# Kernel tuning notes

Hardware: AMD Instinct MI355X
Metric: run time of the kernel (lower is better)

The kernel has to match this reference:

```python
import jax, jax.numpy as jnp
import numpy as np
from functools import partial

NUM_HEADS = 12
NUM_CLUSTERS = 98
LN_EPS = 1e-5
INF = 1e10


def _ln(x, g, b):
    m = x.mean(-1, keepdims=True)
    v = ((x - m) ** 2).mean(-1, keepdims=True)
    return (x - m) / jnp.sqrt(v + LN_EPS) * g + b


def _agglom(dist, num_clusters):
    # dist: [T,T] precomputed distances; average-linkage agglomerative clustering.
    T = dist.shape[0]
    D = dist.at[jnp.arange(T), jnp.arange(T)].set(INF)
    sizes = jnp.ones((T,), dist.dtype)
    labels = jnp.arange(T)
    active = jnp.ones((T,), bool)

    def step(_, state):
        D, sizes, labels, active = state
        Dm = jnp.where(active[:, None] & active[None, :], D, INF)
        idx = jnp.argmin(Dm)
        i0, j0 = idx // T, idx % T
        i = jnp.minimum(i0, j0)
        j = jnp.maximum(i0, j0)
        ni, nj = sizes[i], sizes[j]
        # Lance-Williams update for average linkage
        newd = (ni * D[i] + nj * D[j]) / (ni + nj)
        D = D.at[i, :].set(newd).at[:, i].set(newd)
        D = D.at[i, i].set(INF)
        D = D.at[j, :].set(INF).at[:, j].set(INF)
        sizes = sizes.at[i].set(ni + nj)
        labels = jnp.where(labels == j, i, labels)
        active = active.at[j].set(False)
        return (D, sizes, labels, active)

    D, sizes, labels, active = jax.lax.fori_loop(0, T - num_clusters, step, (D, sizes, labels, active))
    rank = jnp.cumsum(active.astype(jnp.int32)) - 1  # compact active cluster ids to 0..K-1
    return rank[labels]


def reference(x, attn_size, n1_g, n1_b, w_qkv, w_proj, b_proj, n2_g, n2_b, w_fc1, b_fc1, w_fc2, b_fc2):
    B, N, C = x.shape
    H = NUM_HEADS
    hd = C // H
    # --- Attention_ToMe ---
    h = _ln(x, n1_g, n1_b)
    qkv = (h @ w_qkv).reshape(B, N, 3, H, hd).transpose(2, 0, 3, 1, 4)
    q, k, v = qkv[0], qkv[1], qkv[2]
    metric = k.mean(axis=1)  # [B,N,hd]
    attn = jnp.einsum('bhqd,bhkd->bhqk', q, k) * (hd ** -0.5)
    attn = attn + jnp.log(attn_size)[:, None, None, :, 0]  # size bias (log 1 = 0 first block)
    attn = jax.nn.softmax(attn, axis=-1)
    xa = jnp.einsum('bhqk,bhkd->bqhd', attn, v).reshape(B, N, C)
    x = x + xa @ w_proj + b_proj
    # --- agglomerative clustering (no_grad in original) ---
    m = jax.lax.stop_gradient(metric)
    m = m / jnp.linalg.norm(m, axis=-1, keepdims=True)
    dist = 1.0 - jnp.einsum('bnd,bmd->bnm', m, m)[:, 1:, 1:]  # drop cls token
    labels = jax.vmap(partial(_agglom, num_clusters=NUM_CLUSTERS))(dist)  # [B,N-1]
    labels = jnp.concatenate([jnp.zeros((B, 1), labels.dtype), labels + 1], axis=1)  # cls -> cluster 0
    # --- weighted-average merge (scatter_reduce sum expressed as onehot matmul) ---
    Kt = NUM_CLUSTERS + 1
    onehot = (labels[:, :, None] == jnp.arange(Kt)[None, None, :]).astype(x.dtype)  # [B,N,Kt]
    xs = jnp.einsum('bnk,bnc->bkc', onehot, x * attn_size)
    size_new = jnp.einsum('bnk,bnc->bkc', onehot, attn_size)
    x = xs / size_new
    # --- MLP ---
    h = _ln(x, n2_g, n2_b)
    h = jax.nn.gelu(h @ w_fc1 + b_fc1, approximate=False)
    x = x + h @ w_fc2 + b_fc2
    return x, size_new, labels


def setup_inputs() -> dict:
    key = jax.random.key(0)
    ks = jax.random.split(key, 6)
    B, N, C = 64, 197, 768
    Hf = 4 * C
    s = lambda d: 1.0 / np.sqrt(d)
    return {
        'x': jax.random.normal(ks[0], (B, N, C), jnp.float32),
        'attn_size': jnp.ones((B, N, 1), jnp.float32),
        'n1_g': jnp.ones((C,), jnp.float32),
        'n1_b': jnp.zeros((C,), jnp.float32),
        'w_qkv': jax.random.normal(ks[1], (C, 3 * C), jnp.float32) * s(C),
        'w_proj': jax.random.normal(ks[2], (C, C), jnp.float32) * s(C),
        'b_proj': jnp.zeros((C,), jnp.float32),
        'n2_g': jnp.ones((C,), jnp.float32),
        'n2_b': jnp.zeros((C,), jnp.float32),
        'w_fc1': jax.random.normal(ks[3], (C, Hf), jnp.float32) * s(C),
        'b_fc1': jnp.zeros((Hf,), jnp.float32),
        'w_fc2': jax.random.normal(ks[4], (Hf, C), jnp.float32) * s(Hf),
        'b_fc2': jnp.zeros((C,), jnp.float32),
    }
```

## Files before the change

### kernel.cpp

```cpp
#include <hip/hip_runtime.h>
#include <hip/hip_bf16.h>
#include <math.h>

#define INF_ 1e10f
#define LGKM0() asm volatile("s_waitcnt lgkmcnt(0)" ::: "memory")

static constexpr int B_  = 64;
static constexpr int N_  = 197;
static constexpr int C_  = 768;
static constexpr int H_  = 12;
static constexpr int T_  = 196;
static constexpr int KC_ = 98;
static constexpr int KT_ = 99;
static constexpr int HF_ = 3072;

typedef __attribute__((ext_vector_type(8))) short short8v;
typedef __attribute__((ext_vector_type(4))) float f32x4;
typedef __attribute__((ext_vector_type(4))) int int4v;

__device__ __forceinline__ float wave_sum(float v){
#pragma unroll
  for(int o=32;o;o>>=1) v += __shfl_down(v,o);
  return v;
}

__device__ __forceinline__ ushort f2bf(float v){
  __hip_bfloat16 t = __float2bfloat16(v);
  return *reinterpret_cast<const ushort*>(&t);
}

__device__ __forceinline__ unsigned long long packkey(float v, int r, int a){
  unsigned int bb = __float_as_uint(v);
  bb ^= (bb & 0x80000000u) ? 0xFFFFFFFFu : 0x80000000u;
  return ((unsigned long long)bb<<32) | (unsigned)(r<<8) | (unsigned)a;
}
__device__ __forceinline__ float unpackval(unsigned long long key){
  unsigned u = (unsigned)(key>>32);
  u = (u & 0x80000000u) ? (u ^ 0x80000000u) : ~u;
  return __uint_as_float(u);
}

__global__ __launch_bounds__(256) void ln_kernel(const float* __restrict__ in,
    const float* __restrict__ g, const float* __restrict__ bb,
    float* __restrict__ outf, __hip_bfloat16* __restrict__ outb){
  int row = blockIdx.x;
  const float* xr = in + (size_t)row*C_;
  int tid = threadIdx.x;
  float v0=xr[tid], v1=xr[tid+256], v2=xr[tid+512];
  __shared__ float sred[4];
  __shared__ float smean, svar;
  float s = wave_sum(v0+v1+v2);
  int w=tid>>6, l=tid&63;
  if(l==0) sred[w]=s;
  __syncthreads();
  if(tid==0) smean = (sred[0]+sred[1]+sred[2]+sred[3])/(float)C_;
  __syncthreads();
  float m = smean;
  float d0=v0-m, d1=v1-m, d2=v2-m;
  float q = wave_sum(d0*d0+d1*d1+d2*d2);
  if(l==0) sred[w]=q;
  __syncthreads();
  if(tid==0) svar = (sred[0]+sred[1]+sred[2]+sred[3])/(float)C_;
  __syncthreads();
  float sq = sqrtf(svar + 1e-5f);
  float y0 = d0/sq*g[tid]     + bb[tid];
  float y1 = d1/sq*g[tid+256] + bb[tid+256];
  float y2 = d2/sq*g[tid+512] + bb[tid+512];
  if(outf){
    float* orow = outf + (size_t)row*C_;
    orow[tid]=y0; orow[tid+256]=y1; orow[tid+512]=y2;
  }
  if(outb){
    __hip_bfloat16* orow = outb + (size_t)row*C_;
    orow[tid]=__float2bfloat16(y0); orow[tid+256]=__float2bfloat16(y1); orow[tid+512]=__float2bfloat16(y2);
  }
}

__global__ __launch_bounds__(256) void prep_kernel(const float* __restrict__ w_qkv,
    const float* __restrict__ w_proj, const float* __restrict__ w_fc1,
    const float* __restrict__ w_fc2, float* __restrict__ Wm,
    __hip_bfloat16* __restrict__ wqkvT, __hip_bfloat16* __restrict__ wprojT,
    __hip_bfloat16* __restrict__ wfc1T, __hip_bfloat16* __restrict__ wfc2T){
  int bid = blockIdx.x;
  int tid = threadIdx.x;
  if(bid < 192){
    int t = bid*256 + tid;
    if(t >= C_*64) return;
    int c = t>>6, d = t&63;
    const float* p = w_qkv + (size_t)c*(3*C_) + C_ + d;
    float s=0.f;
#pragma unroll
    for(int h=0;h<H_;h++) s += p[h*64];
    Wm[t] = s*(1.0f/12.0f);
    return;
  }
  bid -= 192;
  const float* w; __hip_bfloat16* wt; int K, N, nbx;
  if(bid < 1728){ w=w_qkv; wt=wqkvT; K=C_; N=3*C_; nbx=72; }
  else if(bid < 1728+576){ bid-=1728; w=w_proj; wt=wprojT; K=C_; N=C_; nbx=24; }
  else if(bid < 1728+576+2304){ bid-=1728+576; w=w_fc1; wt=wfc1T; K=C_; N=HF_; nbx=96; }
  else { bid-=1728+576+2304; w=w_fc2; wt=wfc2T; K=HF_; N=C_; nbx=24; }
  __shared__ float tile[32][33];
  int n0 = (bid%nbx)*32, k0 = (bid/nbx)*32;
  int tx = tid&31, ty = tid>>5;
  for(int r=ty;r<32;r+=8) tile[r][tx] = w[(size_t)(k0+r)*N + n0+tx];
  __syncthreads();
  for(int r=ty;r<32;r+=8) wt[(size_t)(n0+r)*K + k0+tx] = __float2bfloat16(tile[tx][r]);
}

template<int EPI>
__global__ __launch_bounds__(256) void gemm_bf16(const ushort* __restrict__ A,
    const ushort* __restrict__ Bt, const float* __restrict__ bias,
    const float* __restrict__ res, void* __restrict__ Cout,
    int M, int N, int K){
  constexpr int BM=128, BN=128, BK=32;
  __shared__ ushort As[BM][BK];
  __shared__ ushort Bs[BN][BK];
  int tid = threadIdx.x;
  int bm = blockIdx.y*BM, bn = blockIdx.x*BN;
  int w = tid>>6, l = tid&63;
  int wm = (w>>1)*64, wn = (w&1)*64;
  int lr = l&15, lc = l>>4;
  f32x4 acc[4][4] = {};
  for(int k0=0;k0<K;k0+=BK){
#pragma unroll
    for(int s=0;s<2;s++){
      int c = s*256 + tid;
      int r = c>>2, q = c&3;
      if(bm + r < M){
        const ushort* srcA = A + (size_t)(bm+r)*K + k0 + q*8;
        __builtin_amdgcn_global_load_lds(
            (const __attribute__((address_space(1))) void*)srcA,
            (__attribute__((address_space(3))) void*)((char*)&As[0][0] + c*16), 16, 0, 0);
      }
      const ushort* srcB = Bt + (size_t)(bn+r)*K + k0 + q*8;
      __builtin_amdgcn_global_load_lds(
          (const __attribute__((address_space(1))) void*)srcB,
          (__attribute__((address_space(3))) void*)((char*)&Bs[0][0] + c*16), 16, 0, 0);
    }
    __syncthreads();
    short8v af[4], bfr[4];
#pragma unroll
    for(int f=0; f<4; f++){
      af[f]  = *reinterpret_cast<const short8v*>(&As[wm + f*16 + lr][lc*8]);
      bfr[f] = *reinterpret_cast<const short8v*>(&Bs[wn + f*16 + lr][lc*8]);
    }
#pragma unroll
    for(int i=0;i<4;i++)
#pragma unroll
      for(int j=0;j<4;j++)
        acc[i][j] = __builtin_amdgcn_mfma_f32_16x16x32_bf16(af[i], bfr[j], acc[i][j], 0,0,0);
    __syncthreads();
  }
#pragma unroll
  for(int i=0;i<4;i++){
    int rbase = bm + wm + i*16 + lc*4;
#pragma unroll
    for(int j=0;j<4;j++){
      int col = bn + wn + j*16 + lr;
#pragma unroll
      for(int r=0;r<4;r++){
        int row = rbase + r;
        if(row >= M) continue;
        size_t idx = (size_t)row*N + col;
        float v = acc[i][j][r];
        if constexpr(EPI==1 || EPI==3) ((float*)Cout)[idx] = (res[idx] + v) + bias[col];
        if constexpr(EPI==2){
          v += bias[col];
          v = 0.5f*v*(1.0f+erff(v*0.70710678118654752f));
          ((__hip_bfloat16*)Cout)[idx] = __float2bfloat16(v);
        }
        if constexpr(EPI==4) ((__hip_bfloat16*)Cout)[idx] = __float2bfloat16(v);
      }
    }
  }
}

__global__ __launch_bounds__(256) void metric_gemm(const float* __restrict__ h,
    const float* __restrict__ Wm, float* __restrict__ mnorm){
  int row0 = blockIdx.x*16;
  __shared__ float hs[16][C_];
  int tid = threadIdx.x;
  int w = tid>>6, l = tid&63;
  for(int t=tid; t<16*C_; t+=256)
    hs[t/C_][t%C_] = h[(size_t)row0*C_ + t];
  __syncthreads();
  float a0=0.f,a1=0.f,a2=0.f,a3=0.f;
#pragma unroll 4
  for(int c=0;c<C_;c++){
    float wv = Wm[c*64+l];
    a0 = fmaf(hs[w*4+0][c], wv, a0);
    a1 = fmaf(hs[w*4+1][c], wv, a1);
    a2 = fmaf(hs[w*4+2][c], wv, a2);
    a3 = fmaf(hs[w*4+3][c], wv, a3);
  }
  float accs[4] = {a0,a1,a2,a3};
#pragma unroll
  for(int r=0;r<4;r++){
    float acc = accs[r];
    float q = acc*acc;
#pragma unroll
    for(int o=32;o;o>>=1) q += __shfl_xor(q,o);
    float nrm = sqrtf(q);
    int row = row0 + w*4 + r;
    int bb = row / N_, n = row - bb*N_;
    if(n>=1) mnorm[((size_t)bb*T_+(n-1))*64+l] = acc/nrm;
  }
}

struct ClusterSh {
  float D[T_][T_+1];
  unsigned long long rowkey[T_];
  unsigned long long gkey[2][4];
  unsigned long long scratch[4];
  float sizes[T_];
  int labels[T_];
  int active[T_];
  int rlist[T_];
  int rcnt;
};
struct AttnSh {
  ushort Ks[208][72];
  ushort VsT[64][232];
  ushort Ps[4][16][232];
  float lsz[208];
};
union FusedSh { ClusterSh c; AttnSh a; };

__device__ void cluster_body(ClusterSh& S, const float* __restrict__ mnorm,
    int* __restrict__ labs_ws, float* __restrict__ labs_out, int b){
  int tid = threadIdx.x;
  int w = tid>>6, l = tid&63;
  const float* mb = mnorm + (size_t)b*T_*64;

  for(int t=tid;t<T_*T_;t+=256){
    int r=t/T_, c=t%T_;
    float dot=0.0f;
    for(int d=0;d<64;d++) dot += mb[r*64+d]*mb[c*64+d];
    S.D[r][c] = (r==c) ? INF_ : (1.0f - dot);
  }
  for(int t=tid;t<T_;t+=256){ S.sizes[t]=1.0f; S.labels[t]=t; S.active[t]=1; }
  if(tid<8) S.gkey[tid>>2][tid&3] = ~0ULL;
  __syncthreads();
  if(tid<T_){
    float bvv=INF_; int ba=0;
    for(int c=0;c<T_;c++){ float v=S.D[tid][c]; if(v<bvv){ bvv=v; ba=c; } }
    S.rowkey[tid] = packkey(bvv, tid, ba);
  }
  __syncthreads();

  for(int it=0; it<T_-KC_; it++){
    int p = it&1;
    unsigned long long key = (tid<T_) ? S.rowkey[tid] : ~0ULL;
    atomicMin(&S.gkey[p][w], key);
    if(tid==0) S.rcnt = 0;
    __syncthreads();
    unsigned long long g0=S.gkey[p][0], g1=S.gkey[p][1];
    unsigned long long g2=S.gkey[p][2], g3=S.gkey[p][3];
    unsigned long long ga = g0<g1?g0:g1, gb2 = g2<g3?g2:g3;
    unsigned long long g  = ga<gb2?ga:gb2;
    int i = (int)((g>>8)&0xFF);
    int j = (int)(g&0xFF);
    float ni = S.sizes[i], nj = S.sizes[j];
    int k=tid;
    if(k<T_){
      float di=S.D[i][k], dj=S.D[j][k];
      unsigned long long oldkey = S.rowkey[k];
      float oldrm = unpackval(oldkey);
      int oldarg = (int)(oldkey & 0xFF);
      bool kact = (k!=i) && (k!=j) && (S.active[k]!=0);
      float nd = kact ? (ni*di + nj*dj) / (ni+nj) : INF_;
      S.D[i][k]=nd; S.D[k][i]=nd; S.D[j][k]=INF_; S.D[k][j]=INF_;
      if(S.labels[k]==j) S.labels[k]=i;
      if(k==i){
        int q=atomicAdd(&S.rcnt,1); S.rlist[q]=k;
      } else if(k==j){
        S.rowkey[k] = packkey(INF_, k, 0);
      } else if(kact){
        if(oldarg==i){
          if(nd<=oldrm) S.rowkey[k] = packkey(nd, k, i);
          else { int q=atomicAdd(&S.rcnt,1); S.rlist[q]=k; }
        } else if(oldarg==j){
          if(nd<=oldrm) S.rowkey[k] = packkey(nd, k, i);
          else { int q=atomicAdd(&S.rcnt,1); S.rlist[q]=k; }
        } else {
          if(nd<oldrm || (nd==oldrm && i<oldarg)) S.rowkey[k] = packkey(nd, k, i);
        }
      }
    }
    if(tid==0){ S.sizes[i]=ni+nj; S.active[j]=0; }
    if(l==0) atomicExch(&S.gkey[p^1][w], ~0ULL);
    __syncthreads();
    int nr = S.rcnt;
    for(int q=w; q<nr; q+=4){
      int rr = S.rlist[q];
      if(l==0) atomicExch(&S.scratch[w], ~0ULL);
      unsigned long long lk = ~0ULL;
      for(int cc=l; cc<T_; cc+=64){
        unsigned long long ck = packkey(S.D[rr][cc], rr, cc);
        if(ck<lk) lk=ck;
      }
      atomicMin(&S.scratch[w], lk);
      LGKM0();
      unsigned long long rk = S.scratch[w];
      if(l==0) S.rowkey[rr] = rk;
    }
    __syncthreads();
  }

  if(tid==0){
    int c=0;
    for(int t=0;t<T_;t++){ c += S.active[t]; S.rlist[t]=c-1; }
    labs_ws[b*N_]=0; labs_out[b*N_]=0.0f;
  }
  __syncthreads();
  for(int t=tid;t<T_;t+=256){
    int lab = S.rlist[S.labels[t]] + 1;
    labs_ws[b*N_+1+t] = lab;
    labs_out[b*N_+1+t] = (float)lab;
  }
}

__device__ void attn_body(AttnSh& S, const ushort* __restrict__ qkv,
    const float* __restrict__ attn_size, __hip_bfloat16* __restrict__ xa, int h, int b){
  int tid = threadIdx.x;
  int w = tid>>6, l = tid&63;
  int lr = l&15, lc = l>>4;
  const size_t QROW = 3*C_;
  for(int t=tid; t<208*64; t+=256){
    int n=t>>6, d=t&63;
    ushort v = 0;
    if(n<197) v = qkv[((size_t)(b*N_+n))*QROW + C_ + h*64 + d];
    S.Ks[n][d] = v;
  }
  for(int t=tid; t<232*64; t+=256){
    int n=t>>6, d=t&63;
    ushort v = 0;
    if(n<197) v = qkv[((size_t)(b*N_+n))*QROW + 2*C_ + h*64 + d];
    S.VsT[d][n] = v;
  }
  for(int t=tid;t<208;t+=256) S.lsz[t] = (t<197)? logf(attn_size[b*N_+t]) : 0.f;
  for(int c=l; c<16*24; c+=64){ int rr=c/24, cc=208+(c%24); S.Ps[w][rr][cc]=0; }
  __syncthreads();

  for(int qt=w; qt<13; qt+=4){
    int qrow = min(qt*16 + lr, 196);
    const ushort* qp = qkv + ((size_t)(b*N_+qrow))*QROW + h*64;
    short8v aq0 = *reinterpret_cast<const short8v*>(qp + lc*8);
    short8v aq1 = *reinterpret_cast<const short8v*>(qp + 32 + lc*8);
    float sc[13][4];
#pragma unroll
    for(int t=0;t<13;t++){
      short8v b0 = *reinterpret_cast<const short8v*>(&S.Ks[t*16+lr][lc*8]);
      short8v b1 = *reinterpret_cast<const short8v*>(&S.Ks[t*16+lr][32+lc*8]);
      f32x4 a = {0.f,0.f,0.f,0.f};
      a = __builtin_amdgcn_mfma_f32_16x16x32_bf16(aq0, b0, a, 0,0,0);
      a = __builtin_amdgcn_mfma_f32_16x16x32_bf16(aq1, b1, a, 0,0,0);
      float ls = S.lsz[t*16+lr];
      bool mask = (t==12) && (lr>=5);
#pragma unroll
      for(int r=0;r<4;r++) sc[t][r] = mask ? -1e30f : (a[r]*0.125f + ls);
    }
    float rsum[4];
#pragma unroll
    for(int r=0;r<4;r++){
      float m=-1e30f;
#pragma unroll
      for(int t=0;t<13;t++) m = fmaxf(m, sc[t][r]);
#pragma unroll
      for(int o=1;o<16;o<<=1) m = fmaxf(m, __shfl_xor(m,o));
      float s=0.f;
#pragma unroll
      for(int t=0;t<13;t++){ float p=expf(sc[t][r]-m); sc[t][r]=p; s+=p; }
#pragma unroll
      for(int o=1;o<16;o<<=1) s += __shfl_xor(s,o);
      rsum[r]=s;
    }
#pragma unroll
    for(int t=0;t<13;t++)
#pragma unroll
      for(int r=0;r<4;r++)
        S.Ps[w][lc*4+r][t*16+lr] = f2bf(sc[t][r]);
    LGKM0();
    short8v ap[7];
#pragma unroll
    for(int ks=0;ks<7;ks++) ap[ks] = *reinterpret_cast<const short8v*>(&S.Ps[w][lr][ks*32 + lc*8]);
#pragma unroll
    for(int f=0; f<4; f++){
      f32x4 o = {0.f,0.f,0.f,0.f};
#pragma unroll
      for(int ks=0;ks<7;ks++){
        short8v bv = *reinterpret_cast<const short8v*>(&S.VsT[f*16+lr][ks*32 + lc*8]);
        o = __builtin_amdgcn_mfma_f32_16x16x32_bf16(ap[ks], bv, o, 0,0,0);
      }
#pragma unroll
      for(int r=0;r<4;r++){
        int q = qt*16 + lc*4 + r;
        if(q<197) xa[((size_t)(b*N_+q))*C_ + h*64 + f*16 + lr] = __float2bfloat16(o[r]/rsum[r]);
      }
    }
  }
}

__global__ __launch_bounds__(256) void cluster_attn_fused(
    const float* __restrict__ mnorm, int* __restrict__ labs_ws, float* __restrict__ labs_out,
    const ushort* __restrict__ qkv, const float* __restrict__ attn_size,
    __hip_bfloat16* __restrict__ xa){
  __shared__ FusedSh sh;
  int bid = blockIdx.x;
  if(bid < B_){
    cluster_body(sh.c, mnorm, labs_ws, labs_out, bid);
  } else {
    int idx = bid - B_;
    attn_body(sh.a, qkv, attn_size, xa, idx % H_, idx / H_);
  }
}

__global__ __launch_bounds__(256) void merge_kernel(const float* __restrict__ x1,
    const float* __restrict__ asz, const int* __restrict__ labs,
    float* __restrict__ x2, float* __restrict__ size_out){
  int chunk = blockIdx.x;
  int b = blockIdx.y;
  __shared__ float acc[KT_][256];
  __shared__ int   lab[N_];
  __shared__ float sz[N_];
  __shared__ float ssum[KT_];
  int tid = threadIdx.x;
  for(int t=tid;t<N_;t+=256){ lab[t]=labs[b*N_+t]; sz[t]=asz[b*N_+t]; }
#pragma unroll
  for(int k=0;k<KT_;k++) acc[k][tid]=0.f;
  __syncthreads();
  if(tid<KT_){
    float s=0.f;
    for(int n=0;n<N_;n++) if(lab[n]==tid) s += sz[n];
    ssum[tid]=s;
  }
  int c = chunk*256 + tid;
  const float* xb = x1 + (size_t)b*N_*C_ + c;
  for(int n=0;n<N_;n++){
    float v = xb[(size_t)n*C_];
    int k = lab[n];
    acc[k][tid] += v * sz[n];
  }
  __syncthreads();
  for(int k=0;k<KT_;k++)
    x2[((size_t)(b*KT_+k))*C_ + c] = acc[k][tid] / ssum[k];
  if(chunk==0 && tid<KT_) size_out[b*KT_+tid] = ssum[tid];
}

extern "C" void kernel_launch(void* const* d_in, const int* in_sizes, int n_in,
                              void* d_out, int out_size, void* d_ws, size_t ws_size,
                              hipStream_t stream){
  const float* x      = (const float*)d_in[0];
  const float* asz    = (const float*)d_in[1];
  const float* n1_g   = (const float*)d_in[2];
  const float* n1_b   = (const float*)d_in[3];
  const float* w_qkv  = (const float*)d_in[4];
  const float* w_proj = (const float*)d_in[5];
  const float* b_proj = (const float*)d_in[6];
  const float* n2_g   = (const float*)d_in[7];
  const float* n2_b   = (const float*)d_in[8];
  const float* w_fc1  = (const float*)d_in[9];
  const float* b_fc1  = (const float*)d_in[10];
  const float* w_fc2  = (const float*)d_in[11];
  const float* b_fc2  = (const float*)d_in[12];

  const size_t ROWS = (size_t)B_*N_;
  const size_t M2   = (size_t)B_*KT_;
  float* ws = (float*)d_ws;

  float* h     = ws;
  float* qkvR  = h + ROWS*C_;
  __hip_bfloat16* qkvb = (__hip_bfloat16*)qkvR;
  float* x2    = qkvR;
  __hip_bfloat16* h2b = (__hip_bfloat16*)(qkvR + M2*C_);
  __hip_bfloat16* h3b = (__hip_bfloat16*)(qkvR + M2*C_ + M2*C_/2);
  __hip_bfloat16* hb  = (__hip_bfloat16*)(qkvR + ROWS*3*C_);
  __hip_bfloat16* xa  = hb;
  float* mnorm = (float*)(hb) + ROWS*C_/2;
  float* Wm    = mnorm + (size_t)B_*T_*64;
  __hip_bfloat16* wqkvT = (__hip_bfloat16*)(Wm + C_*64);
  __hip_bfloat16* wprojT= (__hip_bfloat16*)((float*)wqkvT + (size_t)3*C_*C_/2);
  __hip_bfloat16* wfc1T = (__hip_bfloat16*)((float*)wprojT + (size_t)C_*C_/2);
  __hip_bfloat16* wfc2T = (__hip_bfloat16*)((float*)wfc1T + (size_t)C_*HF_/2);
  int*   labs  = (int*)((float*)wfc2T + (size_t)HF_*C_/2);
  float* x1    = h;

  float* out     = (float*)d_out;
  float* out_sz  = out + M2*C_;
  float* out_lab = out_sz + M2;

  ln_kernel<<<dim3((unsigned)ROWS),256,0,stream>>>(x, n1_g, n1_b, h, hb);
  prep_kernel<<<dim3(192 + 1728 + 576 + 2304 + 2304),256,0,stream>>>(
      w_qkv, w_proj, w_fc1, w_fc2, Wm, wqkvT, wprojT, wfc1T, wfc2T);

  gemm_bf16<4><<<dim3(18,99),256,0,stream>>>((const ushort*)hb, (const ushort*)wqkvT,
      nullptr, nullptr, qkvb, (int)ROWS, 3*C_, C_);
  metric_gemm<<<dim3(788),256,0,stream>>>(h, Wm, mnorm);

  cluster_attn_fused<<<dim3(B_ + H_*B_),256,0,stream>>>(mnorm, labs, out_lab,
      (const ushort*)qkvb, asz, xa);

  gemm_bf16<1><<<dim3(6,99),256,0,stream>>>((const ushort*)xa, (const ushort*)wprojT,
      b_proj, x, x1, (int)ROWS, C_, C_);
  merge_kernel<<<dim3(3,B_),256,0,stream>>>(x1, asz, labs, x2, out_sz);

  ln_kernel<<<dim3((unsigned)M2),256,0,stream>>>(x2, n2_g, n2_b, nullptr, h2b);
  gemm_bf16<2><<<dim3(24,50),256,0,stream>>>((const ushort*)h2b, (const ushort*)wfc1T,
      b_fc1, nullptr, h3b, (int)M2, HF_, C_);
  gemm_bf16<3><<<dim3(6,50),256,0,stream>>>((const ushort*)h3b, (const ushort*)wfc2T,
      b_fc2, x2, out, (int)M2, C_, HF_);
}
```

Measured before the change: 960.0 us.

## Fuse LN with weight prep and build persistent stage with atomic work queues

Merges the first LayerNorm with the weight transpose/prep kernel, and replaces the QKV GEMM, metric GEMM and cluster/attention kernels with a single persistent 256-block kernel that pulls work items through atomic counters. Cluster blocks start as soon as all metric tiles finish, overlapping the long serial clustering with the QKV GEMM and attention. This cuts launches and lets the clustering tail hide behind other work. The cost is spin-waits, atomic traffic, and a shared-memory union that may lower occupancy for the GEMM and attention paths.

```diff
diff --git a/kernel.cpp b/kernel.cpp
--- a/kernel.cpp
+++ b/kernel.cpp
@@ -14,6 +14,12 @@
 static constexpr int KT_ = 99;
 static constexpr int HF_ = 3072;
 
+static constexpr int N_LN1    = B_*N_;
+static constexpr int N_PREP   = 192 + 1728 + 576 + 2304 + 2304;
+static constexpr int N_METRIC = 788;
+static constexpr int N_QKV    = 1782;
+static constexpr int N_ATTN   = 768;
+
 typedef __attribute__((ext_vector_type(8))) short short8v;
 typedef __attribute__((ext_vector_type(4))) float f32x4;
 typedef __attribute__((ext_vector_type(4))) int int4v;
@@ -40,29 +46,27 @@
   return __uint_as_float(u);
 }
 
-__global__ __launch_bounds__(256) void ln_kernel(const float* __restrict__ in,
+__device__ void ln_body(const float* __restrict__ in,
     const float* __restrict__ g, const float* __restrict__ bb,
-    float* __restrict__ outf, __hip_bfloat16* __restrict__ outb){
-  int row = blockIdx.x;
+    float* __restrict__ outf, __hip_bfloat16* __restrict__ outb, int row,
+    float* sred, float* sm2){
+  int tid = threadIdx.x;
   const float* xr = in + (size_t)row*C_;
-  int tid = threadIdx.x;
   float v0=xr[tid], v1=xr[tid+256], v2=xr[tid+512];
-  __shared__ float sred[4];
-  __shared__ float smean, svar;
   float s = wave_sum(v0+v1+v2);
   int w=tid>>6, l=tid&63;
   if(l==0) sred[w]=s;
   __syncthreads();
-  if(tid==0) smean = (sred[0]+sred[1]+sred[2]+sred[3])/(float)C_;
-  __syncthreads();
-  float m = smean;
+  if(tid==0) sm2[0] = (sred[0]+sred[1]+sred[2]+sred[3])/(float)C_;
+  __syncthreads();
+  float m = sm2[0];
   float d0=v0-m, d1=v1-m, d2=v2-m;
   float q = wave_sum(d0*d0+d1*d1+d2*d2);
   if(l==0) sred[w]=q;
   __syncthreads();
-  if(tid==0) svar = (sred[0]+sred[1]+sred[2]+sred[3])/(float)C_;
-  __syncthreads();
-  float sq = sqrtf(svar + 1e-5f);
+  if(tid==0) sm2[1] = (sred[0]+sred[1]+sred[2]+sred[3])/(float)C_;
+  __syncthreads();
+  float sq = sqrtf(sm2[1] + 1e-5f);
   float y0 = d0/sq*g[tid]     + bb[tid];
   float y1 = d1/sq*g[tid+256] + bb[tid+256];
   float y2 = d2/sq*g[tid+512] + bb[tid+512];
@@ -76,13 +80,31 @@
   }
 }
 
-__global__ __launch_bounds__(256) void prep_kernel(const float* __restrict__ w_qkv,
-    const float* __restrict__ w_proj, const float* __restrict__ w_fc1,
-    const float* __restrict__ w_fc2, float* __restrict__ Wm,
-    __hip_bfloat16* __restrict__ wqkvT, __hip_bfloat16* __restrict__ wprojT,
-    __hip_bfloat16* __restrict__ wfc1T, __hip_bfloat16* __restrict__ wfc2T){
+__global__ __launch_bounds__(256) void ln_kernel(const float* __restrict__ in,
+    const float* __restrict__ g, const float* __restrict__ bb,
+    float* __restrict__ outf, __hip_bfloat16* __restrict__ outb){
+  __shared__ float sred[4];
+  __shared__ float sm2[2];
+  ln_body(in, g, bb, outf, outb, blockIdx.x, sred, sm2);
+}
+
+__global__ __launch_bounds__(256) void ln_prep_kernel(const float* __restrict__ x,
+    const float* __restrict__ n1_g, const float* __restrict__ n1_b,
+    float* __restrict__ h, __hip_bfloat16* __restrict__ hb,
+    const float* __restrict__ w_qkv, const float* __restrict__ w_proj,
+    const float* __restrict__ w_fc1, const float* __restrict__ w_fc2,
+    float* __restrict__ Wm, __hip_bfloat16* __restrict__ wqkvT,
+    __hip_bfloat16* __restrict__ wprojT, __hip_bfloat16* __restrict__ wfc1T,
+    __hip_bfloat16* __restrict__ wfc2T, int* __restrict__ ctrs){
+  __shared__ union { struct { float sred[4]; float sm2[2]; } l; float tile[32][33]; } sh;
   int bid = blockIdx.x;
   int tid = threadIdx.x;
+  if(bid < N_LN1){
+    if(bid==0 && tid<8) ctrs[tid]=0;
+    ln_body(x, n1_g, n1_b, h, hb, bid, sh.l.sred, sh.l.sm2);
+    return;
+  }
+  bid -= N_LN1;
   if(bid < 192){
     int t = bid*256 + tid;
     if(t >= C_*64) return;
@@ -90,7 +112,7 @@
     const float* p = w_qkv + (size_t)c*(3*C_) + C_ + d;
     float s=0.f;
 #pragma unroll
-    for(int h=0;h<H_;h++) s += p[h*64];
+    for(int hh=0;hh<H_;hh++) s += p[hh*64];
     Wm[t] = s*(1.0f/12.0f);
     return;
   }
@@ -100,112 +122,11 @@
   else if(bid < 1728+576){ bid-=1728; w=w_proj; wt=wprojT; K=C_; N=C_; nbx=24; }
   else if(bid < 1728+576+2304){ bid-=1728+576; w=w_fc1; wt=wfc1T; K=C_; N=HF_; nbx=96; }
   else { bid-=1728+576+2304; w=w_fc2; wt=wfc2T; K=HF_; N=C_; nbx=24; }
-  __shared__ float tile[32][33];
   int n0 = (bid%nbx)*32, k0 = (bid/nbx)*32;
   int tx = tid&31, ty = tid>>5;
-  for(int r=ty;r<32;r+=8) tile[r][tx] = w[(size_t)(k0+r)*N + n0+tx];
-  __syncthreads();
-  for(int r=ty;r<32;r+=8) wt[(size_t)(n0+r)*K + k0+tx] = __float2bfloat16(tile[tx][r]);
-}
-
-template<int EPI>
-__global__ __launch_bounds__(256) void gemm_bf16(const ushort* __restrict__ A,
-    const ushort* __restrict__ Bt, const float* __restrict__ bias,
-    const float* __restrict__ res, void* __restrict__ Cout,
-    int M, int N, int K){
-  constexpr int BM=128, BN=128, BK=32;
-  __shared__ ushort As[BM][BK];
-  __shared__ ushort Bs[BN][BK];
-  int tid = threadIdx.x;
-  int bm = blockIdx.y*BM, bn = blockIdx.x*BN;
-  int w = tid>>6, l = tid&63;
-  int wm = (w>>1)*64, wn = (w&1)*64;
-  int lr = l&15, lc = l>>4;
-  f32x4 acc[4][4] = {};
-  for(int k0=0;k0<K;k0+=BK){
-#pragma unroll
-    for(int s=0;s<2;s++){
-      int c = s*256 + tid;
-      int r = c>>2, q = c&3;
-      if(bm + r < M){
-        const ushort* srcA = A + (size_t)(bm+r)*K + k0 + q*8;
-        __builtin_amdgcn_global_load_lds(
-            (const __attribute__((address_space(1))) void*)srcA,
-            (__attribute__((address_space(3))) void*)((char*)&As[0][0] + c*16), 16, 0, 0);
-      }
-      const ushort* srcB = Bt + (size_t)(bn+r)*K + k0 + q*8;
-      __builtin_amdgcn_global_load_lds(
-          (const __attribute__((address_space(1))) void*)srcB,
-          (__attribute__((address_space(3))) void*)((char*)&Bs[0][0] + c*16), 16, 0, 0);
-    }
-    __syncthreads();
-    short8v af[4], bfr[4];
-#pragma unroll
-    for(int f=0; f<4; f++){
-      af[f]  = *reinterpret_cast<const short8v*>(&As[wm + f*16 + lr][lc*8]);
-      bfr[f] = *reinterpret_cast<const short8v*>(&Bs[wn + f*16 + lr][lc*8]);
-    }
-#pragma unroll
-    for(int i=0;i<4;i++)
-#pragma unroll
-      for(int j=0;j<4;j++)
-        acc[i][j] = __builtin_amdgcn_mfma_f32_16x16x32_bf16(af[i], bfr[j], acc[i][j], 0,0,0);
-    __syncthreads();
-  }
-#pragma unroll
-  for(int i=0;i<4;i++){
-    int rbase = bm + wm + i*16 + lc*4;
-#pragma unroll
-    for(int j=0;j<4;j++){
-      int col = bn + wn + j*16 + lr;
-#pragma unroll
-      for(int r=0;r<4;r++){
-        int row = rbase + r;
-        if(row >= M) continue;
-        size_t idx = (size_t)row*N + col;
-        float v = acc[i][j][r];
-        if constexpr(EPI==1 || EPI==3) ((float*)Cout)[idx] = (res[idx] + v) + bias[col];
-        if constexpr(EPI==2){
-          v += bias[col];
-          v = 0.5f*v*(1.0f+erff(v*0.70710678118654752f));
-          ((__hip_bfloat16*)Cout)[idx] = __float2bfloat16(v);
-        }
-        if constexpr(EPI==4) ((__hip_bfloat16*)Cout)[idx] = __float2bfloat16(v);
-      }
-    }
-  }
-}
-
-__global__ __launch_bounds__(256) void metric_gemm(const float* __restrict__ h,
-    const float* __restrict__ Wm, float* __restrict__ mnorm){
-  int row0 = blockIdx.x*16;
-  __shared__ float hs[16][C_];
-  int tid = threadIdx.x;
-  int w = tid>>6, l = tid&63;
-  for(int t=tid; t<16*C_; t+=256)
-    hs[t/C_][t%C_] = h[(size_t)row0*C_ + t];
-  __syncthreads();
-  float a0=0.f,a1=0.f,a2=0.f,a3=0.f;
-#pragma unroll 4
-  for(int c=0;c<C_;c++){
-    float wv = Wm[c*64+l];
-    a0 = fmaf(hs[w*4+0][c], wv, a0);
-    a1 = fmaf(hs[w*4+1][c], wv, a1);
-    a2 = fmaf(hs[w*4+2][c], wv, a2);
-    a3 = fmaf(hs[w*4+3][c], wv, a3);
-  }
-  float accs[4] = {a0,a1,a2,a3};
-#pragma unroll
-  for(int r=0;r<4;r++){
-    float acc = accs[r];
-    float q = acc*acc;
-#pragma unroll
-    for(int o=32;o;o>>=1) q += __shfl_xor(q,o);
-    float nrm = sqrtf(q);
-    int row = row0 + w*4 + r;
-    int bb = row / N_, n = row - bb*N_;
-    if(n>=1) mnorm[((size_t)bb*T_+(n-1))*64+l] = acc/nrm;
-  }
+  for(int r=ty;r<32;r+=8) sh.tile[r][tx] = w[(size_t)(k0+r)*N + n0+tx];
+  __syncthreads();
+  for(int r=ty;r<32;r+=8) wt[(size_t)(n0+r)*K + k0+tx] = __float2bfloat16(sh.tile[tx][r]);
 }
 
 struct ClusterSh {
@@ -225,7 +146,196 @@
   ushort Ps[4][16][232];
   float lsz[208];
 };
-union FusedSh { ClusterSh c; AttnSh a; };
+struct GemmSh { ushort As[128][32]; ushort Bs[128][32]; };
+struct MetricSh { float hs[16][C_]; };
+union FusedSh { ClusterSh c; AttnSh a; GemmSh g; MetricSh m; };
+
+template<int EPI>
+__device__ void gemm_body(GemmSh& S, const ushort* __restrict__ A,
+    const ushort* __restrict__ Bt, const float* __restrict__ bias,
+    const float* __restrict__ res, void* __restrict__ Cout,
+    int M, int N, int K, int bx, int by){
+  constexpr int BM=128, BN=128, BK=32;
+  int tid = threadIdx.x;
+  int bm = by*BM, bn = bx*BN;
+  int w = tid>>6, l = tid&63;
+  int wm = (w>>1)*64, wn = (w&1)*64;
+  int lr = l&15, lc = l>>4;
+  f32x4 acc[4][4] = {};
+  for(int k0=0;k0<K;k0+=BK){
+#pragma unroll
+    for(int s=0;s<2;s++){
+      int c = s*256 + tid;
+      int r = c>>2, q = c&3;
+      if(bm + r < M){
+        const ushort* srcA = A + (size_t)(bm+r)*K + k0 + q*8;
+        __builtin_amdgcn_global_load_lds(
+            (const __attribute__((address_space(1))) void*)srcA,
+            (__attribute__((address_space(3))) void*)((char*)&S.As[0][0] + c*16), 16, 0, 0);
+      }
+      const ushort* srcB = Bt + (size_t)(bn+r)*K + k0 + q*8;
+      __builtin_amdgcn_global_load_lds(
+          (const __attribute__((address_space(1))) void*)srcB,
+          (__attribute__((address_space(3))) void*)((char*)&S.Bs[0][0] + c*16), 16, 0, 0);
+    }
+    __syncthreads();
+    short8v af[4], bfr[4];
+#pragma unroll
+    for(int f=0; f<4; f++){
+      af[f]  = *reinterpret_cast<const short8v*>(&S.As[wm + f*16 + lr][lc*8]);
+      bfr[f] = *reinterpret_cast<const short8v*>(&S.Bs[wn + f*16 + lr][lc*8]);
+    }
+#pragma unroll
+    for(int i=0;i<4;i++)
+#pragma unroll
+      for(int j=0;j<4;j++)
+        acc[i][j] = __builtin_amdgcn_mfma_f32_16x16x32_bf16(af[i], bfr[j], acc[i][j], 0,0,0);
+    __syncthreads();
+  }
+#pragma unroll
+  for(int i=0;i<4;i++){
+    int rbase = bm + wm + i*16 + lc*4;
+#pragma unroll
+    for(int j=0;j<4;j++){
+      int col = bn + wn + j*16 + lr;
+#pragma unroll
+      for(int r=0;r<4;r++){
+        int row = rbase + r;
+        if(row >= M) continue;
+        size_t idx = (size_t)row*N + col;
+        float v = acc[i][j][r];
+        if constexpr(EPI==1 || EPI==3) ((float*)Cout)[idx] = (res[idx] + v) + bias[col];
+        if constexpr(EPI==2){
+          v += bias[col];
+          v = 0.5f*v*(1.0f+erff(v*0.70710678118654752f));
+          ((__hip_bfloat16*)Cout)[idx] = __float2bfloat16(v);
+        }
+        if constexpr(EPI==4) ((__hip_bfloat16*)Cout)[idx] = __float2bfloat16(v);
+      }
+    }
+  }
+}
+
+template<int EPI>
+__global__ __launch_bounds__(256) void gemm_bf16(const ushort* __restrict__ A,
+    const ushort* __restrict__ Bt, const float* __restrict__ bias,
+    const float* __restrict__ res, void* __restrict__ Cout,
+    int M, int N, int K){
+  __shared__ GemmSh S;
+  gemm_body<EPI>(S, A, Bt, bias, res, Cout, M, N, K, blockIdx.x, blockIdx.y);
+}
+
+__device__ void metric_body(MetricSh& S, const float* __restrict__ h,
+    const float* __restrict__ Wm, float* __restrict__ mnorm, int item){
+  int row0 = item*16;
+  int tid = threadIdx.x;
+  int w = tid>>6, l = tid&63;
+  for(int t=tid; t<16*C_; t+=256)
+    S.hs[t/C_][t%C_] = h[(size_t)row0*C_ + t];
+  __syncthreads();
+  float a0=0.f,a1=0.f,a2=0.f,a3=0.f;
+#pragma unroll 4
+  for(int c=0;c<C_;c++){
+    float wv = Wm[c*64+l];
+    a0 = fmaf(S.hs[w*4+0][c], wv, a0);
+    a1 = fmaf(S.hs[w*4+1][c], wv, a1);
+    a2 = fmaf(S.hs[w*4+2][c], wv, a2);
+    a3 = fmaf(S.hs[w*4+3][c], wv, a3);
+  }
+  float accs[4] = {a0,a1,a2,a3};
+#pragma unroll
+  for(int r=0;r<4;r++){
+    float acc = accs[r];
+    float q = acc*acc;
+#pragma unroll
+    for(int o=32;o;o>>=1) q += __shfl_xor(q,o);
+    float nrm = sqrtf(q);
+    int row = row0 + w*4 + r;
+    int bb = row / N_, n = row - bb*N_;
+    if(n>=1) mnorm[((size_t)bb*T_+(n-1))*64+l] = acc/nrm;
+  }
+}
+
+__device__ void attn_body(AttnSh& S, const ushort* __restrict__ qkv,
+    const float* __restrict__ attn_size, __hip_bfloat16* __restrict__ xa, int h, int b){
+  int tid = threadIdx.x;
+  int w = tid>>6, l = tid&63;
+  int lr = l&15, lc = l>>4;
+  const size_t QROW = 3*C_;
+  for(int t=tid; t<208*64; t+=256){
+    int n=t>>6, d=t&63;
+    ushort v = 0;
+    if(n<197) v = qkv[((size_t)(b*N_+n))*QROW + C_ + h*64 + d];
+    S.Ks[n][d] = v;
+  }
+  for(int t=tid; t<232*64; t+=256){
+    int n=t>>6, d=t&63;
+    ushort v = 0;
+    if(n<197) v = qkv[((size_t)(b*N_+n))*QROW + 2*C_ + h*64 + d];
+    S.VsT[d][n] = v;
+  }
+  for(int t=tid;t<208;t+=256) S.lsz[t] = (t<197)? logf(attn_size[b*N_+t]) : 0.f;
+  for(int c=l; c<16*24; c+=64){ int rr=c/24, cc=208+(c%24); S.Ps[w][rr][cc]=0; }
+  __syncthreads();
+
+  for(int qt=w; qt<13; qt+=4){
+    int qrow = min(qt*16 + lr, 196);
+    const ushort* qp = qkv + ((size_t)(b*N_+qrow))*QROW + h*64;
+    short8v aq0 = *reinterpret_cast<const short8v*>(qp + lc*8);
+    short8v aq1 = *reinterpret_cast<const short8v*>(qp + 32 + lc*8);
+    float sc[13][4];
+#pragma unroll
+    for(int t=0;t<13;t++){
+      short8v b0 = *reinterpret_cast<const short8v*>(&S.Ks[t*16+lr][lc*8]);
+      short8v b1 = *reinterpret_cast<const short8v*>(&S.Ks[t*16+lr][32+lc*8]);
+      f32x4 a = {0.f,0.f,0.f,0.f};
+      a = __builtin_amdgcn_mfma_f32_16x16x32_bf16(aq0, b0, a, 0,0,0);
+      a = __builtin_amdgcn_mfma_f32_16x16x32_bf16(aq1, b1, a, 0,0,0);
+      float ls = S.lsz[t*16+lr];
+      bool mask = (t==12) && (lr>=5);
+#pragma unroll
+      for(int r=0;r<4;r++) sc[t][r] = mask ? -1e30f : (a[r]*0.125f + ls);
+    }
+    float rsum[4];
+#pragma unroll
+    for(int r=0;r<4;r++){
+      float m=-1e30f;
+#pragma unroll
+      for(int t=0;t<13;t++) m = fmaxf(m, sc[t][r]);
+#pragma unroll
+      for(int o=1;o<16;o<<=1) m = fmaxf(m, __shfl_xor(m,o));
+      float s=0.f;
+#pragma unroll
+      for(int t=0;t<13;t++){ float p=expf(sc[t][r]-m); sc[t][r]=p; s+=p; }
+#pragma unroll
+      for(int o=1;o<16;o<<=1) s += __shfl_xor(s,o);
+      rsum[r]=s;
+    }
+#pragma unroll
+    for(int t=0;t<13;t++)
+#pragma unroll
+      for(int r=0;r<4;r++)
+        S.Ps[w][lc*4+r][t*16+lr] = f2bf(sc[t][r]);
+    LGKM0();
+    short8v ap[7];
+#pragma unroll
+    for(int ks=0;ks<7;ks++) ap[ks] = *reinterpret_cast<const short8v*>(&S.Ps[w][lr][ks*32 + lc*8]);
+#pragma unroll
+    for(int f=0; f<4; f++){
+      f32x4 o = {0.f,0.f,0.f,0.f};
+#pragma unroll
+      for(int ks=0;ks<7;ks++){
+        short8v bv = *reinterpret_cast<const short8v*>(&S.VsT[f*16+lr][ks*32 + lc*8]);
+        o = __builtin_amdgcn_mfma_f32_16x16x32_bf16(ap[ks], bv, o, 0,0,0);
+      }
+#pragma unroll
+      for(int r=0;r<4;r++){
+        int q = qt*16 + lc*4 + r;
+        if(q<197) xa[((size_t)(b*N_+q))*C_ + h*64 + f*16 + lr] = __float2bfloat16(o[r]/rsum[r]);
+      }
+    }
+  }
+}
 
 __device__ void cluster_body(ClusterSh& S, const float* __restrict__ mnorm,
     int* __restrict__ labs_ws, float* __restrict__ labs_out, int b){
@@ -321,98 +431,66 @@
   }
 }
 
-__device__ void attn_body(AttnSh& S, const ushort* __restrict__ qkv,
-    const float* __restrict__ attn_size, __hip_bfloat16* __restrict__ xa, int h, int b){
-  int tid = threadIdx.x;
-  int w = tid>>6, l = tid&63;
-  int lr = l&15, lc = l>>4;
-  const size_t QROW = 3*C_;
-  for(int t=tid; t<208*64; t+=256){
-    int n=t>>6, d=t&63;
-    ushort v = 0;
-    if(n<197) v = qkv[((size_t)(b*N_+n))*QROW + C_ + h*64 + d];
-    S.Ks[n][d] = v;
-  }
-  for(int t=tid; t<232*64; t+=256){
-    int n=t>>6, d=t&63;
-    ushort v = 0;
-    if(n<197) v = qkv[((size_t)(b*N_+n))*QROW + 2*C_ + h*64 + d];
-    S.VsT[d][n] = v;
-  }
-  for(int t=tid;t<208;t+=256) S.lsz[t] = (t<197)? logf(attn_size[b*N_+t]) : 0.f;
-  for(int c=l; c<16*24; c+=64){ int rr=c/24, cc=208+(c%24); S.Ps[w][rr][cc]=0; }
-  __syncthreads();
-
-  for(int qt=w; qt<13; qt+=4){
-    int qrow = min(qt*16 + lr, 196);
-    const ushort* qp = qkv + ((size_t)(b*N_+qrow))*QROW + h*64;
-    short8v aq0 = *reinterpret_cast<const short8v*>(qp + lc*8);
-    short8v aq1 = *reinterpret_cast<const short8v*>(qp + 32 + lc*8);
-    float sc[13][4];
-#pragma unroll
-    for(int t=0;t<13;t++){
-      short8v b0 = *reinterpret_cast<const short8v*>(&S.Ks[t*16+lr][lc*8]);
-      short8v b1 = *reinterpret_cast<const short8v*>(&S.Ks[t*16+lr][32+lc*8]);
-      f32x4 a = {0.f,0.f,0.f,0.f};
-      a = __builtin_amdgcn_mfma_f32_16x16x32_bf16(aq0, b0, a, 0,0,0);
-      a = __builtin_amdgcn_mfma_f32_16x16x32_bf16(aq1, b1, a, 0,0,0);
-      float ls = S.lsz[t*16+lr];
-      bool mask = (t==12) && (lr>=5);
-#pragma unroll
-      for(int r=0;r<4;r++) sc[t][r] = mask ? -1e30f : (a[r]*0.125f + ls);
-    }
-    float rsum[4];
-#pragma unroll
-    for(int r=0;r<4;r++){
-      float m=-1e30f;
-#pragma unroll
-      for(int t=0;t<13;t++) m = fmaxf(m, sc[t][r]);
-#pragma unroll
-      for(int o=1;o<16;o<<=1) m = fmaxf(m, __shfl_xor(m,o));
-      float s=0.f;
-#pragma unroll
-      for(int t=0;t<13;t++){ float p=expf(sc[t][r]-m); sc[t][r]=p; s+=p; }
-#pragma unroll
-      for(int o=1;o<16;o<<=1) s += __shfl_xor(s,o);
-      rsum[r]=s;
-    }
-#pragma unroll
-    for(int t=0;t<13;t++)
-#pragma unroll
-      for(int r=0;r<4;r++)
-        S.Ps[w][lc*4+r][t*16+lr] = f2bf(sc[t][r]);
-    LGKM0();
-    short8v ap[7];
-#pragma unroll
-    for(int ks=0;ks<7;ks++) ap[ks] = *reinterpret_cast<const short8v*>(&S.Ps[w][lr][ks*32 + lc*8]);
-#pragma unroll
-    for(int f=0; f<4; f++){
-      f32x4 o = {0.f,0.f,0.f,0.f};
-#pragma unroll
-      for(int ks=0;ks<7;ks++){
-        short8v bv = *reinterpret_cast<const short8v*>(&S.VsT[f*16+lr][ks*32 + lc*8]);
-        o = __builtin_amdgcn_mfma_f32_16x16x32_bf16(ap[ks], bv, o, 0,0,0);
-      }
-#pragma unroll
-      for(int r=0;r<4;r++){
-        int q = qt*16 + lc*4 + r;
-        if(q<197) xa[((size_t)(b*N_+q))*C_ + h*64 + f*16 + lr] = __float2bfloat16(o[r]/rsum[r]);
-      }
-    }
-  }
-}
-
-__global__ __launch_bounds__(256) void cluster_attn_fused(
-    const float* __restrict__ mnorm, int* __restrict__ labs_ws, float* __restrict__ labs_out,
-    const ushort* __restrict__ qkv, const float* __restrict__ attn_size,
-    __hip_bfloat16* __restrict__ xa){
+__global__ __launch_bounds__(256) void stage2(
+    const float* __restrict__ h, const float* __restrict__ Wm, float* __restrict__ mnorm,
+    const ushort* __restrict__ hb, const ushort* __restrict__ wqkvT,
+    __hip_bfloat16* __restrict__ qkvb,
+    const float* __restrict__ asz, __hip_bfloat16* __restrict__ xa,
+    int* __restrict__ labs_ws, float* __restrict__ labs_out, int* __restrict__ ctrs){
   __shared__ FusedSh sh;
+  __shared__ int slot;
   int bid = blockIdx.x;
+  int tid = threadIdx.x;
+
+  for(;;){
+    if(tid==0) slot = atomicAdd(&ctrs[2],1);
+    __syncthreads();
+    int it = slot;
+    __syncthreads();
+    if(it >= N_METRIC) break;
+    metric_body(sh.m, h, Wm, mnorm, it);
+    __syncthreads();
+    __threadfence();
+    if(tid==0) atomicAdd(&ctrs[0],1);
+    __syncthreads();
+  }
+
   if(bid < B_){
+    if(tid==0){
+      while(atomicAdd(&ctrs[0],0) < N_METRIC) __builtin_amdgcn_s_sleep(8);
+    }
+    __syncthreads();
+    __threadfence();
     cluster_body(sh.c, mnorm, labs_ws, labs_out, bid);
-  } else {
-    int idx = bid - B_;
-    attn_body(sh.a, qkv, attn_size, xa, idx % H_, idx / H_);
+    return;
+  }
+
+  for(;;){
+    if(tid==0) slot = atomicAdd(&ctrs[3],1);
+    __syncthreads();
+    int it = slot;
+    __syncthreads();
+    if(it >= N_QKV) break;
+    gemm_body<4>(sh.g, hb, wqkvT, nullptr, nullptr, qkvb,
+                 B_*N_, 3*C_, C_, it%18, it/18);
+    __syncthreads();
+    __threadfence();
+    if(tid==0) atomicAdd(&ctrs[1],1);
+    __syncthreads();
+  }
+  if(tid==0){
+    while(atomicAdd(&ctrs[1],0) < N_QKV) __builtin_amdgcn_s_sleep(8);
+  }
+  __syncthreads();
+  __threadfence();
+  for(;;){
+    if(tid==0) slot = atomicAdd(&ctrs[4],1);
+    __syncthreads();
+    int it = slot;
+    __syncthreads();
+    if(it >= N_ATTN) break;
+    attn_body(sh.a, (const ushort*)qkvb, asz, xa, it%H_, it/H_);
+    __syncthreads();
   }
 }
 
@@ -484,22 +562,18 @@
   __hip_bfloat16* wfc1T = (__hip_bfloat16*)((float*)wprojT + (size_t)C_*C_/2);
   __hip_bfloat16* wfc2T = (__hip_bfloat16*)((float*)wfc1T + (size_t)C_*HF_/2);
   int*   labs  = (int*)((float*)wfc2T + (size_t)HF_*C_/2);
+  int*   ctrs  = labs + ROWS;
   float* x1    = h;
 
   float* out     = (float*)d_out;
   float* out_sz  = out + M2*C_;
   float* out_lab = out_sz + M2;
 
-  ln_kernel<<<dim3((unsigned)ROWS),256,0,stream>>>(x, n1_g, n1_b, h, hb);
-  prep_kernel<<<dim3(192 + 1728 + 576 + 2304 + 2304),256,0,stream>>>(
-      w_qkv, w_proj, w_fc1, w_fc2, Wm, wqkvT, wprojT, wfc1T, wfc2T);
-
-  gemm_bf16<4><<<dim3(18,99),256,0,stream>>>((const ushort*)hb, (const ushort*)wqkvT,
-      nullptr, nullptr, qkvb, (int)ROWS, 3*C_, C_);
-  metric_gemm<<<dim3(788),256,0,stream>>>(h, Wm, mnorm);
-
-  cluster_attn_fused<<<dim3(B_ + H_*B_),256,0,stream>>>(mnorm, labs, out_lab,
-      (const ushort*)qkvb, asz, xa);
+  ln_prep_kernel<<<dim3(N_LN1 + N_PREP),256,0,stream>>>(x, n1_g, n1_b, h, hb,
+      w_qkv, w_proj, w_fc1, w_fc2, Wm, wqkvT, wprojT, wfc1T, wfc2T, ctrs);
+
+  stage2<<<dim3(256),256,0,stream>>>(h, Wm, mnorm, (const ushort*)hb,
+      (const ushort*)wqkvT, qkvb, asz, xa, labs, out_lab, ctrs);
 
   gemm_bf16<1><<<dim3(6,99),256,0,stream>>>((const ushort*)xa, (const ushort*)wprojT,
       b_proj, x, x1, (int)ROWS, C_, C_);
```

After: 1.203 ms. 25.3% more time.
